# Optimization experiments

Measured on AMD Instinct MI355X. Metric: run time of the kernel, lower is better.

## Reference

```python
import jax, jax.numpy as jnp
import numpy as np

B, W, G, E, NI, K = 2048, 8192, 8, 128, 16, 15


def setup_inputs() -> dict:
    key = jax.random.key(0)
    ks = jax.random.split(key, 12)
    wavelengths_nm = jnp.linspace(300.0, 400.0, W, dtype=jnp.float32)
    # Rayleigh optical depth (Hansen & Travis style approximation), AMF=1 column
    lam_um = wavelengths_nm / 1000.0
    rayleigh_od = (0.008569 * lam_um ** -4
                   * (1.0 + 0.0113 * lam_um ** -2 + 0.00013 * lam_um ** -4)).astype(jnp.float32)
    return {
        "gas_columns": jax.random.uniform(ks[0], (B, G), jnp.float32),
        "instrument_ids": jax.random.randint(ks[1], (B,), 0, NI),
        "nuisance_latent": jax.random.normal(ks[2], (B, G), jnp.float32),
        "air_mass": 1.0 + 2.0 * jax.random.uniform(ks[3], (B,), jnp.float32),
        "wavelengths_nm": wavelengths_nm,
        "absorption": 0.1 * jax.random.uniform(ks[4], (G, W), jnp.float32),
        "continuum_basis": 0.05 * jax.random.normal(ks[5], (G + 1, W), jnp.float32),
        "rayleigh_od": rayleigh_od,
        "embed_table": jax.random.normal(ks[6], (NI, E), jnp.float32),
        "w1": jax.random.normal(ks[7], (E + G, 64), jnp.float32) / np.sqrt(E + G),
        "b1": jnp.zeros((64,), jnp.float32),
        "w2": jax.random.normal(ks[8], (64, 7), jnp.float32) / 8.0,
        "b2": jnp.zeros((7,), jnp.float32),
    }


def _gaussian_kernel(width_px, kernel_size):
    half = (kernel_size - 1) / 2
    pos = jnp.linspace(-half, half, kernel_size, dtype=width_px.dtype)  # [K]
    k = jnp.exp(-0.5 * (pos[None, :] / (width_px[:, None] + 1e-6)) ** 2)  # [B,K]
    return k / k.sum(axis=1, keepdims=True)


def _forward(gas_columns, nuisance_latent, air_mass, wavelengths_nm, absorption,
             continuum_basis, rayleigh_od, embed_table, w1, b1, w2, b2,
             instrument_ids):
    b = gas_columns.shape[0]
    am = air_mass[:, None]                                   # [B,1]
    scaled = gas_columns * am                                # [B,G]
    optical_depth = scaled @ absorption                      # [B,W]
    ones = jnp.ones((b, 1), gas_columns.dtype)
    continuum = jnp.concatenate([gas_columns, ones], axis=1) @ continuum_basis  # [B,W]
    differential = optical_depth + continuum + am * rayleigh_od[None, :]

    # nuisance MLP on [latent, embedding]
    embed = embed_table[instrument_ids]                      # [B,E]
    nin = jnp.concatenate([nuisance_latent, embed], axis=-1)
    h = jax.nn.gelu(nin @ w1 + b1, approximate=False)
    p = h @ w2 + b2                                          # [B,7]

    gain = jax.nn.softplus(p[:, 0]) + 0.001
    offset = p[:, 1]
    woff = 0.05 * jnp.tanh(p[:, 2])
    wscale = 1.0 + 0.005 * jnp.tanh(p[:, 3])
    lsf = jnp.clip(jax.nn.softplus(p[:, 4]) + 0.001, 0.2, 5.0)
    stray = jax.nn.sigmoid(p[:, 5]) * 0.05
    nonlin = 0.02 * jnp.tanh(p[:, 6])

    # per-sample wavelength shift/scale + linear resampling
    new_wl = wavelengths_nm[None, :] * wscale[:, None] + woff[:, None]  # [B,W]
    differential = jax.vmap(lambda wq, d: jnp.interp(wq, wavelengths_nm, d))(new_wl, differential)

    # per-sample Gaussian LSF convolution (replicate padding)
    kernel = _gaussian_kernel(lsf, K)                        # [B,K]
    pad = K // 2
    padded = jnp.pad(differential, ((0, 0), (pad, pad)), mode='edge')  # [B,W+K-1]
    n = differential.shape[1]
    convolved = sum(padded[:, k:k + n] * kernel[:, k:k + 1] for k in range(K))

    counts = jnp.exp(-convolved)
    post = gain[:, None] * counts + offset[:, None]
    total_nl = jnp.clip(nonlin, -0.04, 0.04)                 # instrument nonlinearity = 0
    nl_counts = post + total_nl[:, None] * post ** 2
    total_stray = jnp.clip(stray, 0.0, 0.2)                  # instrument stray = 0
    simulated = (1.0 - total_stray[:, None]) * nl_counts \
        + total_stray[:, None] * nl_counts.mean(axis=1, keepdims=True)
    return simulated


def reference(gas_columns, instrument_ids, nuisance_latent, air_mass,
              wavelengths_nm, absorption, continuum_basis, rayleigh_od,
              embed_table, w1, b1, w2, b2):
    return _forward(gas_columns, nuisance_latent, air_mass, wavelengths_nm,
                    absorption, continuum_basis, rayleigh_od, embed_table,
                    w1, b1, w2, b2, instrument_ids)
```

## Files before the change

kernel.cpp:

```cpp
#include <hip/hip_runtime.h>

#define W_ 8192
#define NBATCH 2048
#define NT 512
#define RPB 2
#define CCH 256
#define NCHW 8
#define IRW 272

typedef unsigned short u16_t;
typedef _Float16 h2v __attribute__((ext_vector_type(2)));

__device__ __forceinline__ u16_t f2h(float x){ _Float16 h=(_Float16)x; return __builtin_bit_cast(u16_t,h); }
__device__ __forceinline__ float h2f(u16_t u){ return (float)__builtin_bit_cast(_Float16,u); }
__device__ __forceinline__ unsigned pk2(float a,float b){ return (unsigned)f2h(a)|((unsigned)f2h(b)<<16); }
__device__ __forceinline__ float dot2u(unsigned a,unsigned b,float c){
#if __has_builtin(__builtin_amdgcn_fdot2)
  return __builtin_amdgcn_fdot2(__builtin_bit_cast(h2v,a),__builtin_bit_cast(h2v,b),c,false);
#else
  h2v ha=__builtin_bit_cast(h2v,a), hb=__builtin_bit_cast(h2v,b);
  return c+(float)ha[0]*(float)hb[0]+(float)ha[1]*(float)hb[1];
#endif
}
__device__ __forceinline__ unsigned pkrtz(float a,float b){
#if __has_builtin(__builtin_amdgcn_cvt_pkrtz)
  return __builtin_bit_cast(unsigned, __builtin_amdgcn_cvt_pkrtz(a,b));
#else
  return pk2(a,b);
#endif
}
__device__ __forceinline__ unsigned alignb(unsigned hi, unsigned lo){
#if __has_builtin(__builtin_amdgcn_alignbit)
  return __builtin_amdgcn_alignbit(hi, lo, 16);
#else
  return (lo >> 16) | (hi << 16);
#endif
}
__device__ __forceinline__ float softplusf(float x){ return fmaxf(x,0.f)+log1pf(expf(-fabsf(x))); }
__device__ __forceinline__ unsigned rflv(unsigned v){
  return (unsigned)__builtin_amdgcn_readfirstlane((int)v);
}
__device__ __forceinline__ float rflvf(float v){
  return __builtin_bit_cast(float, __builtin_amdgcn_readfirstlane(__builtin_bit_cast(int, v)));
}

__global__ __launch_bounds__(256, 2)
void doas_prep(const float* __restrict__ absn, const float* __restrict__ cbn,
               const float* __restrict__ ray, const int* __restrict__ iid,
               const float* __restrict__ nuis, const float* __restrict__ emb,
               const float* __restrict__ w1, const float* __restrict__ b1,
               const float* __restrict__ w2, const float* __restrict__ b2,
               unsigned* __restrict__ Tp, float* __restrict__ params){
  const int tid = threadIdx.x;
  const int b = blockIdx.x;
  __shared__ float hS[4][64];
  __shared__ float pS[4][8];

  if (b < 32){
    const int w = b*256 + tid;
    #pragma unroll
    for (int q=0;q<4;++q) Tp[q*W_+w]     = pk2(absn[(2*q)*W_+w], absn[(2*q+1)*W_+w]);
    #pragma unroll
    for (int q=0;q<4;++q) Tp[(4+q)*W_+w] = pk2(cbn[(2*q)*W_+w],  cbn[(2*q+1)*W_+w]);
    Tp[8*W_+w] = pk2(cbn[8*W_+w], ray[w]);
  }

  {
    const int rl = tid >> 6, j = tid & 63;
    const int r = b*4 + rl;
    const int id = iid[r];
    float acc = b1[j];
    const float* nrow = nuis + (size_t)r * 8;
    #pragma unroll
    for (int i = 0; i < 8; ++i) acc = fmaf(nrow[i], w1[i*64 + j], acc);
    const float* erow = emb + (size_t)id * 128;
    for (int i = 0; i < 128; ++i) acc = fmaf(erow[i], w1[(8+i)*64 + j], acc);
    hS[rl][j] = 0.5f * acc * (1.0f + erff(acc * 0.70710678118654752f));
  }
  __syncthreads();
  if (tid < 4*7){
    const int rl = tid / 7, k = tid % 7;
    float p = b2[k];
    for (int j = 0; j < 64; ++j) p = fmaf(hS[rl][j], w2[j*7+k], p);
    pS[rl][k] = p;
  }
  __syncthreads();
  if (tid < 4){
    const int rl = tid;
    const int r = b*4 + rl;
    float p0=pS[rl][0], p1=pS[rl][1], p2=pS[rl][2], p3=pS[rl][3],
          p4=pS[rl][4], p5=pS[rl][5], p6=pS[rl][6];
    float gainv = softplusf(p0) + 0.001f;
    float offv  = p1;
    float woffv = 0.05f * tanhf(p2);
    float wscv  = 1.0f + 0.005f * tanhf(p3);
    float lsf   = fminf(fmaxf(softplusf(p4) + 0.001f, 0.2f), 5.0f);
    float strv  = fminf(fmaxf((1.0f/(1.0f+expf(-p5))) * 0.05f, 0.0f), 0.2f);
    float nlin  = fminf(fmaxf(0.02f * tanhf(p6), -0.04f), 0.04f);
    float iw = 1.0f/(lsf + 1e-6f);
    float ks[15]; float ksum = 0.f;
    #pragma unroll
    for (int k2=0;k2<15;++k2){ float pp=(float)(k2-7)*iw; float e=expf(-0.5f*pp*pp); ks[k2]=e; ksum+=e; }
    float inv = 1.0f/ksum;
    float* pr = params + (size_t)r*16;
    unsigned* pu = (unsigned*)pr;
    #pragma unroll
    for (int i=0;i<7;++i) pu[i] = pk2(ks[2*i]*inv, ks[2*i+1]*inv);
    pu[7] = pk2(ks[14]*inv, 0.0f);
    pr[9]  = wscv;
    pr[10] = (300.0f*(wscv - 1.0f) + woffv) * (8191.0f/100.0f);
    pr[11] = gainv; pr[12] = offv; pr[13] = nlin; pr[14] = strv;
    pr[15] = 0.f;
  }
}

template<bool CLO, bool CHI>
__device__ __forceinline__ void interp_chunk(int cbase, int l, const unsigned* __restrict__ rU,
                                             unsigned* __restrict__ irowU,
                                             float wscale, float posoff){
  #pragma unroll
  for (int it=0; it<3; ++it){
    const int pi = it*64 + l;
    if (pi < 136){
      float v2[2];
      #pragma unroll
      for (int u=0;u<2;++u){
        int j = cbase + 2*pi + u;
        if (CLO) j = max(j, 0);
        if (CHI) j = min(j, W_-1);
        float pos = fmaf((float)j, wscale, posoff);
        if (CLO) pos = fmaxf(pos, 0.0f);
        if (CHI) pos = fminf(pos, 8191.0f);
        int i0 = (int)pos;
        if (CHI) i0 = min(i0, W_-2);
        const float fr = pos - (float)i0;
        const int m = i0 >> 1;
        const unsigned u0 = rU[m];
        const unsigned u1 = rU[m+1];
        const unsigned hu0 = u0 >> 16;
        const bool odd = (i0 & 1);
        const unsigned ua = odd ? hu0 : u0;
        const unsigned ub = odd ? u1  : hu0;
        const float d0 = h2f((u16_t)ua);
        const float d1 = h2f((u16_t)ub);
        v2[u] = fmaf(fr, d1-d0, d0);
      }
      irowU[pi] = pkrtz(v2[0], v2[1]);
    }
  }
}

__global__ __launch_bounds__(NT, 2)
void doas_main4(const unsigned* __restrict__ Tp, const float* __restrict__ gas,
                const float* __restrict__ air, const float* __restrict__ params,
                float* __restrict__ out){
  __shared__ u16_t rowH[RPB*W_ + 16];
  __shared__ u16_t irowS[8][IRW];
  __shared__ float wsumS[8];

  const int tid = threadIdx.x;
  const int r0 = blockIdx.x * RPB;

  unsigned csg[RPB][9];
  #pragma unroll
  for (int rr=0; rr<RPB; ++rr){
    const float am = air[r0+rr];
    const float* gfp = gas + (size_t)(r0+rr)*8;
    #pragma unroll
    for (int q=0;q<4;++q) csg[rr][q]   = rflv(pk2(gfp[2*q]*am, gfp[2*q+1]*am));
    #pragma unroll
    for (int q=0;q<4;++q) csg[rr][4+q] = rflv(pk2(gfp[2*q],    gfp[2*q+1]));
    csg[rr][8] = rflv(pk2(1.0f, am));
  }

  unsigned* rowHU = (unsigned*)rowH;
  #pragma unroll
  for (int it=0; it<4; ++it){
    const int e0 = it*2048 + tid*4;
    uint4 dq[9];
    #pragma unroll
    for (int q=0;q<9;++q) dq[q] = *(const uint4*)(Tp + q*W_ + e0);
    float a[RPB][4];
    #pragma unroll
    for (int rr=0;rr<RPB;++rr){ a[rr][0]=0.f; a[rr][1]=0.f; a[rr][2]=0.f; a[rr][3]=0.f; }
    #pragma unroll
    for (int q=0;q<9;++q){
      #pragma unroll
      for (int rr=0;rr<RPB;++rr){
        a[rr][0] = dot2u(dq[q].x, csg[rr][q], a[rr][0]);
        a[rr][1] = dot2u(dq[q].y, csg[rr][q], a[rr][1]);
        a[rr][2] = dot2u(dq[q].z, csg[rr][q], a[rr][2]);
        a[rr][3] = dot2u(dq[q].w, csg[rr][q], a[rr][3]);
      }
    }
    #pragma unroll
    for (int rr=0;rr<RPB;++rr){
      uint2 wv = make_uint2(pkrtz(a[rr][0],a[rr][1]), pkrtz(a[rr][2],a[rr][3]));
      *(uint2*)(rowHU + ((rr*W_ + e0) >> 1)) = wv;
    }
  }

  const int wid = tid >> 6, l = tid & 63;
  const int row  = wid >> 2;
  const int sidx = wid & 3;
  const float* pr = params + (size_t)(r0 + row) * 16;
  const unsigned* pu = (const unsigned*)pr;
  unsigned kwp[7];
  #pragma unroll
  for (int i=0;i<7;++i) kwp[i] = rflv(pu[i]);
  const unsigned k14lo = rflv(pu[7]);
  const float wscale = rflvf(pr[9]),  posoff = rflvf(pr[10]);
  const float gainv  = rflvf(pr[11]), offv   = rflvf(pr[12]);
  const float nlin   = rflvf(pr[13]), strv   = rflvf(pr[14]);

  __syncthreads();

  const unsigned* rU = (const unsigned*)(rowH + row*W_);
  u16_t* irow = &irowS[wid][0];
  unsigned* irowU = (unsigned*)irow;
  const int segbase = sidx * 2048;

  float accsum = 0.f;
  unsigned nlp[NCHW][2];

  #pragma unroll
  for (int c = 0; c < NCHW; ++c) {
    const int cs = segbase + c*CCH;
    const int cbase = cs - 8;
    if (sidx == 0 && c == 0)
      interp_chunk<true,false>(cbase, l, rU, irowU, wscale, posoff);
    else if (sidx == 3 && c == NCHW-1)
      interp_chunk<false,true>(cbase, l, rU, irowU, wscale, posoff);
    else
      interp_chunk<false,false>(cbase, l, rU, irowU, wscale, posoff);
    __builtin_amdgcn_wave_barrier();
    {
      const uint2* p2 = (const uint2*)irowU + l;
      const uint2 A = p2[0], B = p2[1], C = p2[2], D = p2[3], E = p2[4];
      unsigned q[10] = {A.x,A.y, B.x,B.y, C.x,C.y, D.x,D.y, E.x,E.y};
      unsigned sh[9];
      #pragma unroll
      for (int m=0;m<9;++m) sh[m] = alignb(q[m+1], q[m]);
      float nlv[4];
      #pragma unroll
      for (int t=0;t<4;++t){
        float cv = 0.f;
        if ((t & 1) == 0){
          const int b0 = t >> 1;
          #pragma unroll
          for (int i=0;i<7;++i) cv = dot2u(sh[b0+i], kwp[i], cv);
          cv = dot2u(sh[b0+7], k14lo, cv);
        } else {
          const int b0 = (t+1) >> 1;
          #pragma unroll
          for (int i=0;i<7;++i) cv = dot2u(q[b0+i], kwp[i], cv);
          cv = dot2u(q[b0+7], k14lo, cv);
        }
        const float counts = __expf(-cv);
        const float post = fmaf(gainv, counts, offv);
        const float v = fmaf(nlin*post, post, post);
        accsum += v;
        nlv[t] = v;
      }
      nlp[c][0] = pkrtz(nlv[0], nlv[1]);
      nlp[c][1] = pkrtz(nlv[2], nlv[3]);
    }
    __builtin_amdgcn_wave_barrier();
  }

  float s = accsum;
  #pragma unroll
  for (int off2 = 32; off2 >= 1; off2 >>= 1) s += __shfl_down(s, off2);
  if (l == 0) wsumS[wid] = s;
  __syncthreads();
  const float meanv = (wsumS[row*4+0]+wsumS[row*4+1]+wsumS[row*4+2]+wsumS[row*4+3])
                      * (1.0f/8192.0f);

  {
    const float aa = 1.0f - strv;
    const float bb = strv * meanv;
    float* orow = out + (size_t)(r0 + row) * W_;
    #pragma unroll
    for (int c = 0; c < NCHW; ++c) {
      const unsigned u0 = nlp[c][0], u1 = nlp[c][1];
      float4 o0;
      o0.x = fmaf(aa, h2f((u16_t)(u0 & 0xffffu)), bb);
      o0.y = fmaf(aa, h2f((u16_t)(u0 >> 16)),     bb);
      o0.z = fmaf(aa, h2f((u16_t)(u1 & 0xffffu)), bb);
      o0.w = fmaf(aa, h2f((u16_t)(u1 >> 16)),     bb);
      *(float4*)(orow + segbase + c*CCH + 4*l) = o0;
    }
  }
}

__global__ __launch_bounds__(256, 2)
void doas_mono(const float* __restrict__ gas, const int* __restrict__ iid,
               const float* __restrict__ nuis, const float* __restrict__ air,
               const float* __restrict__ absn, const float* __restrict__ cbn,
               const float* __restrict__ ray, const float* __restrict__ emb,
               const float* __restrict__ w1, const float* __restrict__ b1,
               const float* __restrict__ w2, const float* __restrict__ b2,
               float* __restrict__ out)
{
  __shared__ u16_t ringS[4][2048];
  __shared__ u16_t irowS2[4][544];
  __shared__ float hS[64];
  __shared__ float pS[8];
  __shared__ float scalS[52];
  __shared__ float wsumS[4];

  const int tid = threadIdx.x;
  const int row = blockIdx.x;

  if (tid < 64) {
    const int j = tid;
    const int id = iid[row];
    float acc = b1[j];
    const float* nrow = nuis + (size_t)row * 8;
    #pragma unroll
    for (int i = 0; i < 8; ++i) acc = fmaf(nrow[i], w1[i*64 + j], acc);
    const float* erow = emb + (size_t)id * 128;
    for (int i = 0; i < 128; ++i) acc = fmaf(erow[i], w1[(8+i)*64 + j], acc);
    hS[j] = 0.5f * acc * (1.0f + erff(acc * 0.70710678118654752f));
  }
  __syncthreads();
  if (tid < 7) {
    float p = b2[tid];
    for (int j = 0; j < 64; ++j) p = fmaf(hS[j], w2[j*7+tid], p);
    pS[tid] = p;
  }
  __syncthreads();
  if (tid == 0) {
    float p0=pS[0], p1=pS[1], p2=pS[2], p3=pS[3], p4=pS[4], p5=pS[5], p6=pS[6];
    float gainv = softplusf(p0) + 0.001f;
    float offv  = p1;
    float woffv = 0.05f * tanhf(p2);
    float wscv  = 1.0f + 0.005f * tanhf(p3);
    float lsf   = fminf(fmaxf(softplusf(p4) + 0.001f, 0.2f), 5.0f);
    float strv  = fminf(fmaxf((1.0f/(1.0f+expf(-p5))) * 0.05f, 0.0f), 0.2f);
    float nlin  = fminf(fmaxf(0.02f * tanhf(p6), -0.04f), 0.04f);
    float iw = 1.0f/(lsf + 1e-6f);
    float ks[15]; float ksum = 0.f;
    #pragma unroll
    for (int k2=0;k2<15;++k2){ float pp=(float)(k2-7)*iw; float e=expf(-0.5f*pp*pp); ks[k2]=e; ksum+=e; }
    float inv = 1.0f/ksum;
    scalS[15] = wscv;
    scalS[16] = (300.0f*(wscv - 1.0f) + woffv) * (8191.0f/100.0f);
    scalS[17] = gainv; scalS[18] = offv; scalS[19] = nlin; scalS[20] = strv;
    scalS[22] = air[row];
    unsigned* su = (unsigned*)scalS;
    #pragma unroll
    for (int i=0;i<7;++i) su[32+i] = pk2(ks[2*i]*inv, ks[2*i+1]*inv);
    su[39] = pk2(ks[14]*inv, 0.0f);
    su[40] = pk2(0.0f, ks[14]*inv);
    #pragma unroll
    for (int g=0; g<8; ++g) scalS[23+g] = gas[(size_t)row*8+g];
  }
  __syncthreads();

  const int wid = tid >> 6, l = tid & 63;
  const int segbase = wid * 2048;
  const unsigned* scalU = (const unsigned*)scalS;
  unsigned kwp[7];
  #pragma unroll
  for (int i=0;i<7;++i) kwp[i] = rflv(scalU[32+i]);
  const unsigned k14lo = rflv(scalU[39]), k14hi = rflv(scalU[40]);
  const float wscale = scalS[15], posoff = scalS[16];
  const float gainv  = scalS[17], offv   = scalS[18];
  const float nlin   = scalS[19], strv   = scalS[20];

  u16_t* ring = &ringS[wid][0];
  unsigned* ringU = (unsigned*)ring;
  u16_t* irow = &irowS2[wid][0];
  unsigned* irowU = (unsigned*)irow;

  auto do_diff = [&](int s){
    const int sbase = segbase - 256 + (s << 9);
    #pragma unroll
    for (int it=0; it<4; ++it){
      const int e0 = sbase + ((it*64 + l) << 1);
      const int eL = min(max(e0, 0), W_-2);
      const float am = scalS[22];
      float a0=0.f, a1=0.f;
      #pragma unroll
      for (int g=0; g<8; ++g){
        const float cg = scalS[23+g];
        const float ca = cg*am;
        a0 = fmaf(ca, absn[g*W_+eL],   a0); a0 = fmaf(cg, cbn[g*W_+eL],   a0);
        a1 = fmaf(ca, absn[g*W_+eL+1], a1); a1 = fmaf(cg, cbn[g*W_+eL+1], a1);
      }
      a0 += cbn[8*W_+eL]   + am*ray[eL];
      a1 += cbn[8*W_+eL+1] + am*ray[eL+1];
      ringU[((unsigned)e0 & 2047) >> 1] = pkrtz(a0, a1);
    }
  };

  float accsum = 0.f;
  unsigned nlp[4][4];

  do_diff(0); do_diff(1);
  __builtin_amdgcn_wave_barrier();

  #pragma unroll
  for (int c = 0; c < 4; ++c) {
    if (c < 3) do_diff(c+2);
    __builtin_amdgcn_wave_barrier();
    {
      const int cbase = segbase + (c << 9) - 8;
      #pragma unroll
      for (int it = 0; it < 5; ++it) {
        const int pi = it*64 + l;
        if (pi < 264) {
          float v2[2];
          #pragma unroll
          for (int u=0; u<2; ++u){
            const int j = cbase + 2*pi + u;
            const int jc = min(max(j, 0), W_-1);
            float pos = fmaf((float)jc, wscale, posoff);
            pos = fminf(fmaxf(pos, 0.0f), 8191.0f);
            const int i0 = min((int)pos, W_-2);
            const float fr = pos - (float)i0;
            const float d0 = h2f(ring[ i0    & 2047]);
            const float d1 = h2f(ring[(i0+1) & 2047]);
            v2[u] = fmaf(fr, d1-d0, d0);
          }
          irowU[pi] = pkrtz(v2[0], v2[1]);
        }
      }
    }
    __builtin_amdgcn_wave_barrier();
    {
      const uint4* qp = (const uint4*)irow + l;
      const uint4 A = qp[0], B = qp[1], C = qp[2];
      unsigned q[12] = {A.x,A.y,A.z,A.w, B.x,B.y,B.z,B.w, C.x,C.y,C.z,C.w};
      unsigned sh[10];
      #pragma unroll
      for (int m=0;m<10;++m) sh[m] = alignb(q[m+1], q[m]);
      float nlv[8];
      #pragma unroll
      for (int t=0;t<8;++t){
        const int s2 = t >> 1;
        float cv = 0.f;
        if ((t & 1) == 0){
          #pragma unroll
          for (int i=0;i<7;++i) cv = dot2u(sh[s2+i], kwp[i], cv);
          cv = dot2u(q[s2+7], k14hi, cv);
        } else {
          #pragma unroll
          for (int i=0;i<7;++i) cv = dot2u(q[s2+1+i], kwp[i], cv);
          cv = dot2u(q[s2+8], k14lo, cv);
        }
        const float counts = __expf(-cv);
        const float post = fmaf(gainv, counts, offv);
        const float v = fmaf(nlin*post, post, post);
        accsum += v;
        nlv[t] = v;
      }
      nlp[c][0] = pkrtz(nlv[0], nlv[1]);
      nlp[c][1] = pkrtz(nlv[2], nlv[3]);
      nlp[c][2] = pkrtz(nlv[4], nlv[5]);
      nlp[c][3] = pkrtz(nlv[6], nlv[7]);
    }
    __builtin_amdgcn_wave_barrier();
  }

  float s = accsum;
  #pragma unroll
  for (int off2 = 32; off2 >= 1; off2 >>= 1) s += __shfl_down(s, off2);
  if (l == 0) wsumS[wid] = s;
  __syncthreads();
  const float meanv = (wsumS[0]+wsumS[1]+wsumS[2]+wsumS[3]) * (1.0f/8192.0f);

  {
    const float aa = 1.0f - strv;
    const float bb = strv * meanv;
    float* orow = out + (size_t)row * W_;
    #pragma unroll
    for (int c = 0; c < 4; ++c) {
      const unsigned u0 = nlp[c][0], u1 = nlp[c][1], u2 = nlp[c][2], u3 = nlp[c][3];
      float4 o0, o1;
      o0.x = fmaf(aa, h2f((u16_t)(u0 & 0xffffu)), bb);
      o0.y = fmaf(aa, h2f((u16_t)(u0 >> 16)),     bb);
      o0.z = fmaf(aa, h2f((u16_t)(u1 & 0xffffu)), bb);
      o0.w = fmaf(aa, h2f((u16_t)(u1 >> 16)),     bb);
      o1.x = fmaf(aa, h2f((u16_t)(u2 & 0xffffu)), bb);
      o1.y = fmaf(aa, h2f((u16_t)(u2 >> 16)),     bb);
      o1.z = fmaf(aa, h2f((u16_t)(u3 & 0xffffu)), bb);
      o1.w = fmaf(aa, h2f((u16_t)(u3 >> 16)),     bb);
      float* dst = orow + segbase + (c << 9) + 8*l;
      *(float4*)(dst)     = o0;
      *(float4*)(dst + 4) = o1;
    }
  }
}

extern "C" void kernel_launch(void* const* d_in, const int* in_sizes, int n_in,
                              void* d_out, int out_size, void* d_ws, size_t ws_size,
                              hipStream_t stream) {
  const float* gas  = (const float*)d_in[0];
  const int*   iid  = (const int*)d_in[1];
  const float* nuis = (const float*)d_in[2];
  const float* air  = (const float*)d_in[3];
  const float* wl   = (const float*)d_in[4];
  const float* absn = (const float*)d_in[5];
  const float* cbn  = (const float*)d_in[6];
  const float* ray  = (const float*)d_in[7];
  const float* emb  = (const float*)d_in[8];
  const float* w1   = (const float*)d_in[9];
  const float* b1   = (const float*)d_in[10];
  const float* w2   = (const float*)d_in[11];
  const float* b2   = (const float*)d_in[12];
  float* out = (float*)d_out;
  (void)in_sizes; (void)n_in; (void)out_size; (void)wl;

  const size_t packBytes = (size_t)9 * W_ * 4;
  const size_t parBytes  = (size_t)NBATCH * 16 * 4;

  if (ws_size >= packBytes + parBytes) {
    unsigned* Tp  = (unsigned*)d_ws;
    float* params = (float*)((char*)d_ws + packBytes);
    hipLaunchKernelGGL(doas_prep, dim3(NBATCH/4), dim3(256), 0, stream,
                       absn, cbn, ray, iid, nuis, emb, w1, b1, w2, b2, Tp, params);
    hipLaunchKernelGGL(doas_main4, dim3(NBATCH/RPB), dim3(NT), 0, stream,
                       Tp, gas, air, params, out);
  } else {
    hipLaunchKernelGGL(doas_mono, dim3(NBATCH), dim3(256), 0, stream,
                       gas, iid, nuis, air, absn, cbn, ray, emb, w1, b1, w2, b2, out);
  }
}
```

Measured before the change: 52.95 us.

## Give each wave a private haloed row segment, one row per block

```diff
diff --git a/kernel.cpp b/kernel.cpp
--- a/kernel.cpp
+++ b/kernel.cpp
@@ -2,8 +2,11 @@
 
 #define W_ 8192
 #define NBATCH 2048
-#define NT 512
-#define RPB 2
+#define NT 256
+#define NWAVE 4
+#define SEGW 2048
+#define HALO 192
+#define RWN (SEGW + 2*HALO)
 #define CCH 256
 #define NCHW 8
 #define IRW 272
@@ -115,7 +118,8 @@
 }
 
 template<bool CLO, bool CHI>
-__device__ __forceinline__ void interp_chunk(int cbase, int l, const unsigned* __restrict__ rU,
+__device__ __forceinline__ void interp_chunk(int cbase, int base, int l,
+                                             const unsigned* __restrict__ rWU,
                                              unsigned* __restrict__ irowU,
                                              float wscale, float posoff){
   #pragma unroll
@@ -134,11 +138,12 @@
         int i0 = (int)pos;
         if (CHI) i0 = min(i0, W_-2);
         const float fr = pos - (float)i0;
-        const int m = i0 >> 1;
-        const unsigned u0 = rU[m];
-        const unsigned u1 = rU[m+1];
+        const int li = i0 - base;
+        const int m = li >> 1;
+        const unsigned u0 = rWU[m];
+        const unsigned u1 = rWU[m+1];
         const unsigned hu0 = u0 >> 16;
-        const bool odd = (i0 & 1);
+        const bool odd = (li & 1);
         const unsigned ua = odd ? hu0 : u0;
         const unsigned ub = odd ? u1  : hu0;
         const float d0 = h2f((u16_t)ua);
@@ -151,59 +156,31 @@
 }
 
 __global__ __launch_bounds__(NT, 2)
-void doas_main4(const unsigned* __restrict__ Tp, const float* __restrict__ gas,
+void doas_main6(const unsigned* __restrict__ Tp, const float* __restrict__ gas,
                 const float* __restrict__ air, const float* __restrict__ params,
                 float* __restrict__ out){
-  __shared__ u16_t rowH[RPB*W_ + 16];
-  __shared__ u16_t irowS[8][IRW];
-  __shared__ float wsumS[8];
+  __shared__ u16_t rowW[NWAVE][RWN + 8];
+  __shared__ u16_t irowS[NWAVE][IRW];
+  __shared__ float wsumS[NWAVE];
 
   const int tid = threadIdx.x;
-  const int r0 = blockIdx.x * RPB;
-
-  unsigned csg[RPB][9];
-  #pragma unroll
-  for (int rr=0; rr<RPB; ++rr){
-    const float am = air[r0+rr];
-    const float* gfp = gas + (size_t)(r0+rr)*8;
-    #pragma unroll
-    for (int q=0;q<4;++q) csg[rr][q]   = rflv(pk2(gfp[2*q]*am, gfp[2*q+1]*am));
-    #pragma unroll
-    for (int q=0;q<4;++q) csg[rr][4+q] = rflv(pk2(gfp[2*q],    gfp[2*q+1]));
-    csg[rr][8] = rflv(pk2(1.0f, am));
-  }
-
-  unsigned* rowHU = (unsigned*)rowH;
-  #pragma unroll
-  for (int it=0; it<4; ++it){
-    const int e0 = it*2048 + tid*4;
-    uint4 dq[9];
-    #pragma unroll
-    for (int q=0;q<9;++q) dq[q] = *(const uint4*)(Tp + q*W_ + e0);
-    float a[RPB][4];
-    #pragma unroll
-    for (int rr=0;rr<RPB;++rr){ a[rr][0]=0.f; a[rr][1]=0.f; a[rr][2]=0.f; a[rr][3]=0.f; }
-    #pragma unroll
-    for (int q=0;q<9;++q){
-      #pragma unroll
-      for (int rr=0;rr<RPB;++rr){
-        a[rr][0] = dot2u(dq[q].x, csg[rr][q], a[rr][0]);
-        a[rr][1] = dot2u(dq[q].y, csg[rr][q], a[rr][1]);
-        a[rr][2] = dot2u(dq[q].z, csg[rr][q], a[rr][2]);
-        a[rr][3] = dot2u(dq[q].w, csg[rr][q], a[rr][3]);
-      }
-    }
-    #pragma unroll
-    for (int rr=0;rr<RPB;++rr){
-      uint2 wv = make_uint2(pkrtz(a[rr][0],a[rr][1]), pkrtz(a[rr][2],a[rr][3]));
-      *(uint2*)(rowHU + ((rr*W_ + e0) >> 1)) = wv;
-    }
-  }
-
+  const int row = blockIdx.x;
   const int wid = tid >> 6, l = tid & 63;
-  const int row  = wid >> 2;
-  const int sidx = wid & 3;
-  const float* pr = params + (size_t)(r0 + row) * 16;
+  const int segbase = wid * SEGW;
+  const int base = segbase - HALO;
+
+  unsigned csg[9];
+  {
+    const float am = air[row];
+    const float* gfp = gas + (size_t)row * 8;
+    #pragma unroll
+    for (int q=0;q<4;++q) csg[q]   = rflv(pk2(gfp[2*q]*am, gfp[2*q+1]*am));
+    #pragma unroll
+    for (int q=0;q<4;++q) csg[4+q] = rflv(pk2(gfp[2*q],    gfp[2*q+1]));
+    csg[8] = rflv(pk2(1.0f, am));
+  }
+
+  const float* pr = params + (size_t)row * 16;
   const unsigned* pu = (const unsigned*)pr;
   unsigned kwp[7];
   #pragma unroll
@@ -213,12 +190,25 @@
   const float gainv  = rflvf(pr[11]), offv   = rflvf(pr[12]);
   const float nlin   = rflvf(pr[13]), strv   = rflvf(pr[14]);
 
-  __syncthreads();
-
-  const unsigned* rU = (const unsigned*)(rowH + row*W_);
+  unsigned* rWU = (unsigned*)&rowW[wid][0];
+  #pragma unroll
+  for (int it=0; it<19; ++it){
+    const int idx = it*64 + l;
+    const int e0 = base + 2*idx;
+    const int eL = min(max(e0, 0), W_-2);
+    float a0=0.f, a1=0.f;
+    #pragma unroll
+    for (int q=0;q<9;++q){
+      uint2 d = *(const uint2*)(Tp + q*W_ + eL);
+      a0 = dot2u(d.x, csg[q], a0);
+      a1 = dot2u(d.y, csg[q], a1);
+    }
+    rWU[idx] = pkrtz(a0, a1);
+  }
+  __builtin_amdgcn_wave_barrier();
+
   u16_t* irow = &irowS[wid][0];
   unsigned* irowU = (unsigned*)irow;
-  const int segbase = sidx * 2048;
 
   float accsum = 0.f;
   unsigned nlp[NCHW][2];
@@ -227,12 +217,12 @@
   for (int c = 0; c < NCHW; ++c) {
     const int cs = segbase + c*CCH;
     const int cbase = cs - 8;
-    if (sidx == 0 && c == 0)
-      interp_chunk<true,false>(cbase, l, rU, irowU, wscale, posoff);
-    else if (sidx == 3 && c == NCHW-1)
-      interp_chunk<false,true>(cbase, l, rU, irowU, wscale, posoff);
+    if (wid == 0 && c == 0)
+      interp_chunk<true,false>(cbase, base, l, rWU, irowU, wscale, posoff);
+    else if (wid == NWAVE-1 && c == NCHW-1)
+      interp_chunk<false,true>(cbase, base, l, rWU, irowU, wscale, posoff);
     else
-      interp_chunk<false,false>(cbase, l, rU, irowU, wscale, posoff);
+      interp_chunk<false,false>(cbase, base, l, rWU, irowU, wscale, posoff);
     __builtin_amdgcn_wave_barrier();
     {
       const uint2* p2 = (const uint2*)irowU + l;
@@ -273,13 +263,12 @@
   for (int off2 = 32; off2 >= 1; off2 >>= 1) s += __shfl_down(s, off2);
   if (l == 0) wsumS[wid] = s;
   __syncthreads();
-  const float meanv = (wsumS[row*4+0]+wsumS[row*4+1]+wsumS[row*4+2]+wsumS[row*4+3])
-                      * (1.0f/8192.0f);
+  const float meanv = (wsumS[0]+wsumS[1]+wsumS[2]+wsumS[3]) * (1.0f/8192.0f);
 
   {
     const float aa = 1.0f - strv;
     const float bb = strv * meanv;
-    float* orow = out + (size_t)(r0 + row) * W_;
+    float* orow = out + (size_t)row * W_;
     #pragma unroll
     for (int c = 0; c < NCHW; ++c) {
       const unsigned u0 = nlp[c][0], u1 = nlp[c][1];
@@ -521,7 +510,7 @@
     float* params = (float*)((char*)d_ws + packBytes);
     hipLaunchKernelGGL(doas_prep, dim3(NBATCH/4), dim3(256), 0, stream,
                        absn, cbn, ray, iid, nuis, emb, w1, b1, w2, b2, Tp, params);
-    hipLaunchKernelGGL(doas_main4, dim3(NBATCH/RPB), dim3(NT), 0, stream,
+    hipLaunchKernelGGL(doas_main6, dim3(NBATCH), dim3(NT), 0, stream,
                        Tp, gas, air, params, out);
   } else {
     hipLaunchKernelGGL(doas_mono, dim3(NBATCH), dim3(256), 0, stream,
```

Result: slower. 65.88 us (+24.4%).
